# Kernel tuning notes

Hardware: AMD Instinct MI355X
Metric: run time of the kernel (lower is better)

The kernel has to match this reference:

```python
import jax, jax.numpy as jnp
import numpy as np
from jax import lax

IMG_SIZE = 512
STRIDE = 16
NUM_ANCHORS = 5
NUM_CLASSES = 80
TOPK = 1000
CONF_THRESH = 0.05
NMS_THRESH = 0.6
ANCHOR_SIZE = [[32, 32], [64, 64], [128, 96], [96, 128], [256, 256]]
B = 32
FMP = IMG_SIZE // STRIDE          # 32
M = FMP * FMP * NUM_ANCHORS       # 5120


def _make_anchors():
    # mirrors YOWO.generate_anchors: grid xy (in pixels) + per-cell anchor wh
    ys, xs = jnp.meshgrid(jnp.arange(FMP), jnp.arange(FMP), indexing='ij')
    xy = jnp.stack([xs, ys], axis=-1).astype(jnp.float32).reshape(-1, 2)   # [HW,2]
    xy = jnp.repeat(xy[:, None, :], NUM_ANCHORS, axis=1) * STRIDE          # [HW,A,2]
    wh = jnp.broadcast_to(jnp.asarray(ANCHOR_SIZE, jnp.float32)[None],
                          (FMP * FMP, NUM_ANCHORS, 2))                     # [HW,A,2]
    return jnp.concatenate([xy, wh], axis=-1).reshape(-1, 4)               # [M,4]


def setup_inputs() -> dict:
    key = jax.random.key(0)
    k1, k2, k3 = jax.random.split(key, 3)
    return {
        'conf_pred': jax.random.normal(k1, (B, M, 1), jnp.float32),
        'cls_pred': jax.random.normal(k2, (B, M, NUM_CLASSES), jnp.float32),
        'reg_pred': jax.random.normal(k3, (B, M, 4), jnp.float32),
        'anchor_boxes': _make_anchors(),
    }


def _decode_bbox(anchors, reg_pred):
    # anchors/reg_pred: [..., 4] -> xyxy boxes in pixels
    xy = jax.nn.sigmoid(reg_pred[..., :2]) * STRIDE + anchors[..., :2]
    wh = jnp.exp(reg_pred[..., 2:]) * anchors[..., 2:]
    return jnp.concatenate([xy - 0.5 * wh, xy + 0.5 * wh], axis=-1)


def _pairwise_iou(boxes):
    # boxes: [K,4] xyxy -> [K,K] IoU with the exact epsilons of YOWO.nms
    x1, y1, x2, y2 = boxes[:, 0], boxes[:, 1], boxes[:, 2], boxes[:, 3]
    areas = (x2 - x1) * (y2 - y1)
    xx1 = jnp.maximum(x1[:, None], x1[None, :])
    yy1 = jnp.maximum(y1[:, None], y1[None, :])
    xx2 = jnp.minimum(x2[:, None], x2[None, :])
    yy2 = jnp.minimum(y2[:, None], y2[None, :])
    w = jnp.maximum(1e-28, xx2 - xx1)
    h = jnp.maximum(1e-28, yy2 - yy1)
    inter = w * h
    return inter / (areas[:, None] + areas[None, :] - inter + 1e-14)


def _sequential_nms_keep(iou):
    # boxes assumed sorted by descending score; greedy sequential suppression
    K = iou.shape[0]
    idx = jnp.arange(K)

    def body(i, keep):
        sup = (iou[i] > NMS_THRESH) & (idx > i) & keep[i]
        return keep & ~sup

    return lax.fori_loop(0, K, body, jnp.ones(K, bool))


def reference(conf_pred, cls_pred, reg_pred, anchor_boxes):
    # scoring: sigmoid(obj) * softmax(cls), max over classes  -> [B,M]
    score_all = jax.nn.sigmoid(conf_pred) * jax.nn.softmax(cls_pred, axis=-1)
    scores = jnp.max(score_all, axis=-1)
    labels = jnp.argmax(score_all, axis=-1)

    # topk (lax.top_k returns scores sorted descending)  -> [B,TOPK]
    scores, idx = lax.top_k(scores, TOPK)
    labels = jnp.take_along_axis(labels, idx, axis=1)
    reg_sel = jnp.take_along_axis(reg_pred, idx[..., None], axis=1)
    anc_sel = anchor_boxes[idx]                                   # [B,TOPK,4]

    bboxes = jnp.clip(_decode_bbox(anc_sel, reg_sel) / IMG_SIZE, 0.0, 1.0)

    # per-class NMS via class-offset trick (boxes in [0,1], offset 2.0 per class)
    boxes_off = bboxes + 2.0 * labels.astype(bboxes.dtype)[..., None]
    iou = jax.vmap(_pairwise_iou)(boxes_off)                      # [B,TOPK,TOPK]
    nms_keep = jax.vmap(_sequential_nms_keep)(iou)                # [B,TOPK] bool

    keep = nms_keep & (scores >= CONF_THRESH)
    scores_out = jnp.where(keep, scores, 0.0)
    return scores_out, labels, bboxes, keep
```

## Files before the change

kernel.cpp:

```cpp
#include <hip/hip_runtime.h>
#include <cstdint>
#include <math.h>


constexpr int B = 32;
constexpr int M = 5120;
constexpr int C = 80;
constexpr int K = 1000;
constexpr float NMS_T  = 0.6f;

constexpr int OFF_SCORE = 0;
constexpr int OFF_LAB   = B * K;
constexpr int OFF_BOX   = 2 * B * K;
constexpr int OFF_KEEP  = 2 * B * K + 4 * B * K;

constexpr size_t WS_KEYS     = 0;
constexpr size_t WS_LABELS   = WS_KEYS   + (size_t)B * M * 8;
constexpr size_t WS_SELSC    = WS_LABELS + (size_t)B * M * 4;
constexpr size_t WS_BOXOFF   = WS_SELSC + (size_t)B * K * 4;
constexpr size_t WS_MASK     = WS_BOXOFF + (size_t)B * K * 4 * 4;

__device__ __forceinline__ float expf_cr(float x) {
    return (float)exp((double)x);
}
__device__ __forceinline__ float sigm_np(float x) {
    float e = expf_cr(-x);
    return __fdiv_rn(1.0f, __fadd_rn(1.0f, e));
}

__global__ void __launch_bounds__(256)
k_scores(const float* __restrict__ conf, const float* __restrict__ cls,
         unsigned long long* __restrict__ keys, int* __restrict__ labels) {
    int b = blockIdx.y;
    int g0 = blockIdx.x * 32;
    int tid = threadIdx.x;
    __shared__ float s_lds[32];
    if (tid < 32) {
        s_lds[tid] = sigm_np(conf[(size_t)b * M + g0 + tid]);
    }
    __syncthreads();
    int grp = tid >> 3;
    int j   = tid & 7;
    int m = g0 + grp;
    size_t base = ((size_t)b * M + m) * C + j;
    float x[10];
#pragma unroll
    for (int k = 0; k < 10; k++) x[k] = cls[base + 8 * k];
    float mx = x[0];
#pragma unroll
    for (int k = 1; k < 10; k++) mx = fmaxf(mx, x[k]);
#pragma unroll
    for (int d = 1; d < 8; d <<= 1) mx = fmaxf(mx, __shfl_xor(mx, d, 64));
    float e[10];
#pragma unroll
    for (int k = 0; k < 10; k++) e[k] = expf_cr(__fsub_rn(x[k], mx));
    float r = e[0];
#pragma unroll
    for (int k = 1; k < 10; k++) r = __fadd_rn(r, e[k]);
    float t1  = __fadd_rn(r,  __shfl_xor(r, 1, 64));
    float t2  = __fadd_rn(t1, __shfl_xor(t1, 2, 64));
    float sum = __fadd_rn(t2, __shfl_xor(t2, 4, 64));
    float s = s_lds[grp];
    float best = -1.0f; int bc = 0;
#pragma unroll
    for (int k = 0; k < 10; k++) {
        float q = __fdiv_rn(e[k], sum);
        float p = __fmul_rn(s, q);
        if (p > best) { best = p; bc = 8 * k + j; }
    }
#pragma unroll
    for (int d = 1; d < 8; d <<= 1) {
        float op = __shfl_xor(best, d, 64);
        int   oc = __shfl_xor(bc,   d, 64);
        if (op > best || (op == best && oc < bc)) { best = op; bc = oc; }
    }
    if (j == 0) {
        keys[(size_t)b * M + m] =
            ((unsigned long long)__float_as_uint(best) << 32) |
            (unsigned long long)(0xFFFFFFFFu - (unsigned)m);
        labels[(size_t)b * M + m] = bc;
    }
}

__device__ __forceinline__ void decode_write(
    int b, int rank, int m, float score, int lab,
    const float* __restrict__ reg, const float* __restrict__ anchors,
    float* __restrict__ out, float4* __restrict__ boxes_off,
    float* __restrict__ sel_score)
{
    float4 r = ((const float4*)reg)[(size_t)b * M + m];
    float4 a = ((const float4*)anchors)[m];
    float cx = __fadd_rn(__fmul_rn(sigm_np(r.x), 16.0f), a.x);
    float cy = __fadd_rn(__fmul_rn(sigm_np(r.y), 16.0f), a.y);
    float w  = __fmul_rn(expf_cr(r.z), a.z);
    float h  = __fmul_rn(expf_cr(r.w), a.w);
    float x1 = __fdiv_rn(__fsub_rn(cx, __fmul_rn(0.5f, w)), 512.0f);
    float y1 = __fdiv_rn(__fsub_rn(cy, __fmul_rn(0.5f, h)), 512.0f);
    float x2 = __fdiv_rn(__fadd_rn(cx, __fmul_rn(0.5f, w)), 512.0f);
    float y2 = __fdiv_rn(__fadd_rn(cy, __fmul_rn(0.5f, h)), 512.0f);
    x1 = fminf(fmaxf(x1, 0.0f), 1.0f);
    y1 = fminf(fmaxf(y1, 0.0f), 1.0f);
    x2 = fminf(fmaxf(x2, 0.0f), 1.0f);
    y2 = fminf(fmaxf(y2, 0.0f), 1.0f);
    ((float4*)(out + OFF_BOX))[b * K + rank] = make_float4(x1, y1, x2, y2);
    out[OFF_LAB + b * K + rank] = (float)lab;
    float off = __fmul_rn(2.0f, (float)lab);
    boxes_off[b * K + rank] = make_float4(__fadd_rn(x1, off), __fadd_rn(y1, off),
                                          __fadd_rn(x2, off), __fadd_rn(y2, off));
    sel_score[b * K + rank] = score;
}

__global__ void __launch_bounds__(1024)
k_topk(const unsigned long long* __restrict__ keys,
       const int* __restrict__ labels,
       const float* __restrict__ reg, const float* __restrict__ anchors,
       float* __restrict__ out, float4* __restrict__ boxes_off,
       float* __restrict__ sel_score) {
    int b = blockIdx.x;
    int tid = threadIdx.x;
    const unsigned long long* kb = keys + (size_t)b * M;

    __shared__ unsigned int hist[2048];
    __shared__ unsigned int sufA[2048];
    __shared__ unsigned int sufB[2048];
    __shared__ unsigned long long cand[2048];
    __shared__ int scnt, thrBin, ovf;

    for (int i = tid; i < 2048; i += 1024) hist[i] = 0;
    if (tid == 0) { scnt = 0; ovf = 0; }
    __syncthreads();

    unsigned long long k5[5];
#pragma unroll
    for (int i = 0; i < 5; i++) {
        k5[i] = kb[tid + i * 1024];
        atomicAdd(&hist[(unsigned)(k5[i] >> 51)], 1u);
    }
    __syncthreads();
    for (int i = tid; i < 2048; i += 1024) sufA[i] = hist[i];
    __syncthreads();
    unsigned int* src = sufA; unsigned int* dst = sufB;
    for (int d = 1; d < 2048; d <<= 1) {
        for (int i = tid; i < 2048; i += 1024) {
            unsigned int v = src[i];
            if (i + d < 2048) v += src[i + d];
            dst[i] = v;
        }
        __syncthreads();
        unsigned int* tmp = src; src = dst; dst = tmp;
    }
    for (int i = tid; i < 2048; i += 1024) {
        unsigned int s = src[i];
        unsigned int sn = (i + 1 < 2048) ? src[i + 1] : 0u;
        if (s >= (unsigned)K && sn < (unsigned)K) thrBin = i;
    }
    __syncthreads();
    int T = thrBin;
#pragma unroll
    for (int i = 0; i < 5; i++) {
        if ((int)(k5[i] >> 51) >= T) {
            int pos = atomicAdd(&scnt, 1);
            if (pos < 2048) cand[pos] = k5[i]; else ovf = 1;
        }
    }
    __syncthreads();
    if (!ovf) {
        int S = scnt;
        int N = (S <= 1024) ? 1024 : 2048;
        for (int i = tid; i < 2048; i += 1024)
            if (i >= S) cand[i] = 0ull;
        __syncthreads();
        for (int ksz = 2; ksz <= N; ksz <<= 1) {
            for (int jsz = ksz >> 1; jsz > 0; jsz >>= 1) {
                if (tid < (N >> 1)) {
                    int i = 2 * tid - (tid & (jsz - 1));
                    unsigned long long a = cand[i], c = cand[i + jsz];
                    bool desc = ((i & ksz) == 0);
                    if ((a < c) == desc) { cand[i] = c; cand[i + jsz] = a; }
                }
                __syncthreads();
            }
        }
        if (tid < K) {
            unsigned long long key = cand[tid];
            int mm = (int)(0xFFFFFFFFu - (unsigned)(key & 0xFFFFFFFFu));
            float sc = __uint_as_float((unsigned)(key >> 32));
            int lab = labels[(size_t)b * M + mm];
            decode_write(b, tid, mm, sc, lab, reg, anchors, out, boxes_off, sel_score);
        }
    } else {
#pragma unroll
        for (int i = 0; i < 5; i++) {
            unsigned long long my = k5[i];
            int rank = 0;
            for (int j = 0; j < M; j++) rank += (kb[j] > my) ? 1 : 0;
            if (rank < K) {
                int mm = tid + i * 1024;
                float sc = __uint_as_float((unsigned)(my >> 32));
                int lab = labels[(size_t)b * M + mm];
                decode_write(b, rank, mm, sc, lab, reg, anchors, out, boxes_off, sel_score);
            }
        }
    }
}

__global__ void __launch_bounds__(256)
k_mask(const float4* __restrict__ boxes_off,
       unsigned long long* __restrict__ mask) {
    int b = blockIdx.z;
    int rowTile = blockIdx.x;
    int wgGroup = blockIdx.y;
    if (4 * wgGroup > rowTile) return;
    int tid = threadIdx.x;
    __shared__ float4 sbj[256];
    __shared__ float  saj[256];
    __shared__ float4 sbi[64];
    __shared__ float  sai[64];
    int j = wgGroup * 256 + tid;
    float4 bx = (j < K) ? boxes_off[b * K + j]
                        : make_float4(3e30f, 3e30f, -3e30f, -3e30f);
    sbj[tid] = bx;
    saj[tid] = __fmul_rn(__fsub_rn(bx.z, bx.x), __fsub_rn(bx.w, bx.y));
    if (tid < 64) {
        int i = rowTile * 64 + tid;
        float4 bv = (i < K) ? boxes_off[b * K + i] : make_float4(0, 0, 0, 0);
        sbi[tid] = bv;
        sai[tid] = __fmul_rn(__fsub_rn(bv.z, bv.x), __fsub_rn(bv.w, bv.y));
    }
    __syncthreads();
    int r  = tid & 63;
    int wg = tid >> 6;
    int W  = wgGroup * 4 + wg;
    if (W > rowTile) return;
    int i = rowTile * 64 + r;
    if (i >= K) return;
    float4 bi = sbi[r];
    float ai = sai[r];
    unsigned long long bits = 0ull;
    int base = wg * 64;
#pragma unroll 8
    for (int jj = 0; jj < 64; jj++) {
        float4 bj = sbj[base + jj];
        float xx1 = fmaxf(bi.x, bj.x), yy1 = fmaxf(bi.y, bj.y);
        float xx2 = fminf(bi.z, bj.z), yy2 = fminf(bi.w, bj.w);
        float ww = fmaxf(1e-28f, __fsub_rn(xx2, xx1));
        float hh = fmaxf(1e-28f, __fsub_rn(yy2, yy1));
        float inter = __fmul_rn(ww, hh);
        float denom = __fadd_rn(__fsub_rn(__fadd_rn(ai, saj[base + jj]), inter), 1e-14f);
        float iou = __fdiv_rn(inter, denom);
        if (iou > NMS_T) bits |= (1ull << jj);
    }
    mask[((size_t)b * K + i) * 16 + W] = bits;
}

__global__ void __launch_bounds__(1024)
k_nms(const unsigned long long* __restrict__ mask,
      const float* __restrict__ sel_score,
      float* __restrict__ out) {
    int b = blockIdx.x;
    int j = threadIdx.x;
    int w = j >> 6;
    int jb = j & 63;
    __shared__ unsigned long long U[16], L[16];
    __shared__ int flag[2];
    unsigned long long rw[16];
    if (j < K) {
        const ulonglong2* rp2 =
            (const ulonglong2*)(mask + ((size_t)b * K + j) * 16);
#pragma unroll
        for (int t = 0; t < 8; t++) {
            ulonglong2 v = rp2[t];
            rw[2 * t] = v.x; rw[2 * t + 1] = v.y;
        }
#pragma unroll
        for (int t = 0; t < 16; t++) {
            unsigned long long bm =
                (t < w) ? ~0ull
                        : ((t == w && jb != 0) ? ((1ull << jb) - 1ull) : 0ull);
            rw[t] &= bm;
        }
    } else {
#pragma unroll
        for (int t = 0; t < 16; t++) rw[t] = 0ull;
    }
    if (j < 16) { U[j] = (j < 15) ? ~0ull : ((1ull << 40) - 1); L[j] = 0ull; }
    if (j == 0) { flag[0] = 0; flag[1] = 0; }
    __syncthreads();
    for (int k = 0; k < 1025; k++) {
        unsigned long long supU = 0ull, supL = 0ull;
#pragma unroll
        for (int t = 0; t < 16; t++) {
            unsigned long long Ut = U[t], Lt = L[t];
            supU |= Lt & rw[t];
            supL |= Ut & rw[t];
        }
        bool nu = (j < K) && (supU == 0ull);
        bool nl = (j < K) && (supL == 0ull);
        __syncthreads();
        unsigned long long bu = __ballot(nu);
        unsigned long long bl = __ballot(nl);
        if (jb == 0) {
            U[w] = bu; L[w] = bl;
            if (bu != bl) flag[k & 1] = 1;
        }
        if (j == 0) flag[(k + 1) & 1] = 0;
        __syncthreads();
        if (flag[k & 1] == 0) break;
    }
    if (j < K) {
        bool kp = ((U[w] >> jb) & 1ull) != 0ull;
        float s = sel_score[b * K + j];
        kp = kp && (s >= 0.05f);
        out[OFF_SCORE + b * K + j] = kp ? s : 0.0f;
        out[OFF_KEEP + b * K + j]  = kp ? 1.0f : 0.0f;
    }
}

extern "C" void kernel_launch(void* const* d_in, const int* in_sizes, int n_in,
                              void* d_out, int out_size, void* d_ws, size_t ws_size,
                              hipStream_t stream) {
    const float* conf    = (const float*)d_in[0];
    const float* cls     = (const float*)d_in[1];
    const float* reg     = (const float*)d_in[2];
    const float* anchors = (const float*)d_in[3];
    float* out = (float*)d_out;
    char* ws = (char*)d_ws;

    unsigned long long* keys = (unsigned long long*)(ws + WS_KEYS);
    int*    labels   = (int*)(ws + WS_LABELS);
    float*  sel_sc   = (float*)(ws + WS_SELSC);
    float4* boxes_off = (float4*)(ws + WS_BOXOFF);
    unsigned long long* mask = (unsigned long long*)(ws + WS_MASK);

    k_scores<<<dim3(160, B), 256, 0, stream>>>(conf, cls, keys, labels);
    k_topk  <<<B, 1024, 0, stream>>>(keys, labels, reg, anchors, out, boxes_off, sel_sc);
    k_mask  <<<dim3(16, 4, B), 256, 0, stream>>>(boxes_off, mask);
    k_nms   <<<32, 1024, 0, stream>>>(mask, sel_sc, out);
}
```

Baseline: 158.3 us.

## Use wave-shuffle suffix scan and register bitonic stages in top-k kernel

Replaces the shared-memory Hillis-Steele suffix scan over the 2048-bin histogram with a two-level wavefront shuffle scan, which cuts about a dozen block-wide barriers down to a few. The bitonic sort now does every compare-exchange stage with stride below 64 in registers using xor shuffles, so barriers are needed only for the cross-wave strides. The goal is to reduce barrier and LDS traffic in the per-batch top-k block. The cost is more complex indexing, and correctness depends on the shuffle direction logic matching the original descending order.

```diff
diff --git a/kernel.cpp b/kernel.cpp
--- a/kernel.cpp
+++ b/kernel.cpp
@@ -110,6 +110,12 @@
     sel_score[b * K + rank] = score;
 }
 
+__device__ __forceinline__ void cx_reg(unsigned long long& v, int i, int jsz, int ksz) {
+    unsigned long long vp = __shfl_xor(v, jsz, 64);
+    bool takeMax = (((i & ksz) == 0) == ((i & jsz) == 0));
+    v = takeMax ? (vp > v ? vp : v) : (vp < v ? vp : v);
+}
+
 __global__ void __launch_bounds__(1024)
 k_topk(const unsigned long long* __restrict__ keys,
        const int* __restrict__ labels,
@@ -118,12 +124,13 @@
        float* __restrict__ sel_score) {
     int b = blockIdx.x;
     int tid = threadIdx.x;
+    int lane = tid & 63;
+    int wv   = tid >> 6;
     const unsigned long long* kb = keys + (size_t)b * M;
 
     __shared__ unsigned int hist[2048];
-    __shared__ unsigned int sufA[2048];
-    __shared__ unsigned int sufB[2048];
     __shared__ unsigned long long cand[2048];
+    __shared__ unsigned int waveSuf[17];
     __shared__ int scnt, thrBin, ovf;
 
     for (int i = tid; i < 2048; i += 1024) hist[i] = 0;
@@ -137,22 +144,35 @@
         atomicAdd(&hist[(unsigned)(k5[i] >> 51)], 1u);
     }
     __syncthreads();
-    for (int i = tid; i < 2048; i += 1024) sufA[i] = hist[i];
-    __syncthreads();
-    unsigned int* src = sufA; unsigned int* dst = sufB;
-    for (int d = 1; d < 2048; d <<= 1) {
-        for (int i = tid; i < 2048; i += 1024) {
-            unsigned int v = src[i];
-            if (i + d < 2048) v += src[i + d];
-            dst[i] = v;
-        }
-        __syncthreads();
-        unsigned int* tmp = src; src = dst; dst = tmp;
-    }
-    for (int i = tid; i < 2048; i += 1024) {
-        unsigned int s = src[i];
-        unsigned int sn = (i + 1 < 2048) ? src[i + 1] : 0u;
-        if (s >= (unsigned)K && sn < (unsigned)K) thrBin = i;
+
+    unsigned h0 = hist[2 * tid], h1 = hist[2 * tid + 1];
+    unsigned pr = h0 + h1;
+    unsigned s = pr;
+#pragma unroll
+    for (int d = 1; d < 64; d <<= 1) {
+        unsigned o = __shfl_down(s, d, 64);
+        if (lane + d < 64) s += o;
+    }
+    if (lane == 0) waveSuf[wv] = s;
+    if (tid == 0) waveSuf[16] = 0;
+    __syncthreads();
+    if (wv == 0) {
+        unsigned t = (lane < 16) ? waveSuf[lane] : 0u;
+#pragma unroll
+        for (int d = 1; d < 16; d <<= 1) {
+            unsigned o = __shfl_down(t, d, 64);
+            if (lane + d < 64) t += o;
+        }
+        if (lane < 16) waveSuf[lane] = t;
+    }
+    __syncthreads();
+    {
+        unsigned aboveWave = waveSuf[wv + 1];
+        unsigned aboveLane = s - pr;
+        unsigned suf1 = aboveWave + aboveLane + h1;
+        unsigned suf0 = suf1 + h0;
+        if (suf0 >= (unsigned)K && suf0 - h0 < (unsigned)K) thrBin = 2 * tid;
+        if (suf1 >= (unsigned)K && suf1 - h1 < (unsigned)K) thrBin = 2 * tid + 1;
     }
     __syncthreads();
     int T = thrBin;
@@ -170,8 +190,23 @@
         for (int i = tid; i < 2048; i += 1024)
             if (i >= S) cand[i] = 0ull;
         __syncthreads();
-        for (int ksz = 2; ksz <= N; ksz <<= 1) {
-            for (int jsz = ksz >> 1; jsz > 0; jsz >>= 1) {
+        bool act = (128 * wv < N);
+        int i0 = 128 * wv + lane, i1 = i0 + 64;
+        unsigned long long v0 = 0ull, v1 = 0ull;
+        if (act) { v0 = cand[i0]; v1 = cand[i1]; }
+        if (act) {
+#pragma unroll
+            for (int ksz = 2; ksz <= 64; ksz <<= 1)
+#pragma unroll
+                for (int jsz = ksz >> 1; jsz > 0; jsz >>= 1) {
+                    cx_reg(v0, i0, jsz, ksz);
+                    cx_reg(v1, i1, jsz, ksz);
+                }
+            cand[i0] = v0; cand[i1] = v1;
+        }
+        __syncthreads();
+        for (int ksz = 128; ksz <= N; ksz <<= 1) {
+            for (int jsz = ksz >> 1; jsz >= 64; jsz >>= 1) {
                 if (tid < (N >> 1)) {
                     int i = 2 * tid - (tid & (jsz - 1));
                     unsigned long long a = cand[i], c = cand[i + jsz];
@@ -180,6 +215,16 @@
                 }
                 __syncthreads();
             }
+            if (act) {
+                v0 = cand[i0]; v1 = cand[i1];
+#pragma unroll
+                for (int jsz = 32; jsz > 0; jsz >>= 1) {
+                    cx_reg(v0, i0, jsz, ksz);
+                    cx_reg(v1, i1, jsz, ksz);
+                }
+                cand[i0] = v0; cand[i1] = v1;
+            }
+            __syncthreads();
         }
         if (tid < K) {
             unsigned long long key = cand[tid];
```

After: 155.7 us. No clear change (-1.7%).
